# Kernel tuning notes

Measured on AMD Instinct MI355X. Metric: run time of the kernel, lower is better.

## Reference

```python
import jax, jax.numpy as jnp
import numpy as np

N_NODES = 100000


def gcn_conv(x, W, b, src, tgt, n_nodes):
    """PyG GCNConv: add self-loops, symmetric deg^-1/2 normalization, then aggregate."""
    xw = x @ W  # [N, out]
    # degree including self-loop (edge weights are all 1)
    deg = jnp.zeros((n_nodes,), dtype=x.dtype).at[tgt].add(1.0) + 1.0
    dinv = deg ** -0.5
    norm = dinv[src] * dinv[tgt]  # [E]
    agg = jax.ops.segment_sum(xw[src] * norm[:, None], tgt, num_segments=n_nodes)
    # self-loop contribution: norm_ii = dinv_i^2
    return agg + xw * (dinv ** 2)[:, None] + b


def setup_inputs() -> dict:
    key = jax.random.key(0)
    ks = jax.random.split(key, 9)
    d_in, d_hid, d_out = 128, 128, 64
    x = jax.random.normal(ks[0], (N_NODES, d_in), dtype=jnp.float32)
    edge_index = jax.random.randint(ks[1], (2, 200000), 0, N_NODES)
    pos_edge_index = jax.random.randint(ks[2], (2, 500000), 0, N_NODES)
    s = lambda k, shape, fan: jax.random.normal(k, shape, dtype=jnp.float32) / np.sqrt(fan)
    return {
        "x": x,
        "edge_index": edge_index,
        "pos_edge_index": pos_edge_index,
        "W_init": s(ks[3], (d_in, d_in), d_in),
        "b_init": jnp.zeros((d_in,), dtype=jnp.float32),
        "W1": s(ks[4], (d_in, d_hid), d_in),
        "b1": jnp.zeros((d_hid,), dtype=jnp.float32),
        "W2": s(ks[5], (d_hid, d_out), d_hid),
        "b2": jnp.zeros((d_out,), dtype=jnp.float32),
    }


def reference(x, edge_index, pos_edge_index, W_init, b_init, W1, b1, W2, b2):
    n = x.shape[0]
    src, tgt = pos_edge_index[0], pos_edge_index[1]
    h = x @ W_init + b_init                      # init_linear
    h = gcn_conv(h, W1, b1, src, tgt, n)         # conv1
    h = jax.nn.relu(h)
    h = gcn_conv(h, W2, b2, src, tgt, n)         # conv2
    # edge dot-product scoring (use_bilinear=False)
    logits = jnp.sum(h[edge_index[0]] * h[edge_index[1]], axis=-1)  # [E_pred]
    return logits
```

## Files before the change

### kernel.cpp

```cpp
#include <hip/hip_runtime.h>


typedef __attribute__((ext_vector_type(8))) short short8;
typedef __attribute__((ext_vector_type(4))) float f32x4;

__device__ __forceinline__ ushort f2bf(float v) {
    unsigned u = __float_as_uint(v);
    return (ushort)((u + 0x7FFFu + ((u >> 16) & 1u)) >> 16);
}
__device__ __forceinline__ float bf2f(ushort b) {
    return __uint_as_float(((unsigned)b) << 16);
}
__device__ __forceinline__ float bflo(unsigned u) { return __uint_as_float(u << 16); }
__device__ __forceinline__ float bfhi(unsigned u) { return __uint_as_float(u & 0xFFFF0000u); }
__device__ __forceinline__ unsigned packbf(float x, float y) {
    return (unsigned)f2bf(x) | ((unsigned)f2bf(y) << 16);
}
__device__ __forceinline__ void split2(float v, ushort& h, ushort& l) {
    unsigned u = __float_as_uint(v);
    unsigned hb = (u + 0x7FFFu + ((u >> 16) & 1u)) & 0xFFFF0000u;
    h = (ushort)(hb >> 16);
    l = f2bf(v - __uint_as_float(hb));
}

__global__ void prep_kernel(const float* __restrict__ Wi, const float* __restrict__ W1,
                            const float* __restrict__ W2,
                            ushort* __restrict__ Ti, ushort* __restrict__ T1,
                            ushort* __restrict__ T2, int* __restrict__ zp, int ztot)
{
    int o = blockIdx.x * blockDim.x + threadIdx.x;
    if (o < ztot) zp[o] = 0;
    if (o < 16384) {
        int c = o >> 7, k = o & 127;
        Ti[o] = f2bf(Wi[(size_t)k * 128 + c]);
    } else if (o < 32768) {
        int p = o - 16384;
        int c = p >> 7, k = p & 127;
        T1[p] = f2bf(W1[(size_t)k * 128 + c]);
    } else if (o < 40960) {
        int p = o - 32768;
        int c = p >> 7, k = p & 127;
        T2[p] = f2bf(W2[(size_t)k * 64 + c]);
    }
}

__global__ void hist_kernel(const int* __restrict__ tgt, int* __restrict__ counts, int e) {
    int i = blockIdx.x * blockDim.x + threadIdx.x;
    if (i < e) atomicAdd(&counts[tgt[i]], 1);
}
__global__ __launch_bounds__(256)
void scan1_kernel(const int* __restrict__ counts, int* __restrict__ rowptr,
                  int* __restrict__ bsum, float* __restrict__ dinv, int n)
{
    __shared__ int sdata[256];
    const int t = threadIdx.x;
    const int base = blockIdx.x * 1024 + t * 4;
    int v[4];
#pragma unroll
    for (int i = 0; i < 4; i++) v[i] = (base + i < n) ? counts[base + i] : 0;
#pragma unroll
    for (int i = 0; i < 4; i++)
        if (base + i < n) dinv[base + i] = 1.0f / sqrtf((float)(v[i] + 1));
    int tsum = v[0] + v[1] + v[2] + v[3];
    sdata[t] = tsum;
    __syncthreads();
    for (int off = 1; off < 256; off <<= 1) {
        int x = (t >= off) ? sdata[t - off] : 0;
        __syncthreads();
        if (t >= off) sdata[t] += x;
        __syncthreads();
    }
    if (t == 255) bsum[blockIdx.x] = sdata[255];
    int run = sdata[t] - tsum;
#pragma unroll
    for (int i = 0; i < 4; i++) {
        if (base + i < n) rowptr[base + i] = run;
        run += v[i];
    }
}
__global__ __launch_bounds__(256)
void scan2_kernel(int* __restrict__ bsum, int nb)
{
    __shared__ int sdata[256];
    const int t = threadIdx.x;
    int v = (t < nb) ? bsum[t] : 0;
    sdata[t] = v;
    __syncthreads();
    for (int off = 1; off < 256; off <<= 1) {
        int x = (t >= off) ? sdata[t - off] : 0;
        __syncthreads();
        if (t >= off) sdata[t] += x;
        __syncthreads();
    }
    if (t < nb) bsum[t] = sdata[t] - v;
}
__global__ void scan3_kernel(int* __restrict__ rowptr, const int* __restrict__ bsum,
                             int n, int e_total)
{
    int i = blockIdx.x * blockDim.x + threadIdx.x;
    if (i < n) rowptr[i] += bsum[i >> 10];
    if (i == 0) rowptr[n] = e_total;
}
__global__ void scatter_kernel(const int* __restrict__ src, const int* __restrict__ tgt,
                               const float* __restrict__ dinv, const int* __restrict__ rowptr,
                               int* __restrict__ cursor, int2* __restrict__ ew, int e)
{
    int i = blockIdx.x * blockDim.x + threadIdx.x;
    if (i >= e) return;
    int s = src[i], t = tgt[i];
    int p = rowptr[t] + atomicAdd(&cursor[t], 1);
    ew[p] = make_int2(s, __float_as_int(dinv[s] * dinv[t]));
}

__global__ __launch_bounds__(256)
void fused_gemm01_kernel(const float* __restrict__ x,
                         const ushort* __restrict__ WTi, const ushort* __restrict__ WT1,
                         const float* __restrict__ bias, ushort* __restrict__ xw1, int M)
{
    __shared__ ushort raw[20480];
    ushort (*H0)[128][8] = (ushort(*)[128][8])raw;
    ushort (*Ah)[128][8] = (ushort(*)[128][8])raw;
    ushort (*Al)[128][8] = (ushort(*)[128][8])(raw + 4096);
    ushort (*Bs)[128][8] = (ushort(*)[128][8])(raw + 16384);

    const int tid = threadIdx.x;
    const int row0 = blockIdx.x * 128;
    const int wv = tid >> 6;
    const int l  = tid & 63;
    const int lr = l & 15;
    const int lk = l >> 4;

    f32x4 acc0[8], acc1[8];
#pragma unroll
    for (int n = 0; n < 8; ++n) {
        acc0[n] = (f32x4){0.f, 0.f, 0.f, 0.f};
        acc1[n] = (f32x4){0.f, 0.f, 0.f, 0.f};
    }

    for (int kk = 0; kk < 128; kk += 32) {
        {
            const int r  = tid >> 1;
            const int kh = tid & 1;
            const int gr = row0 + r;
            float f[16];
            if (gr < M) {
                const float4* p = (const float4*)(x + (size_t)gr * 128 + kk + kh * 16);
                float4 q0 = p[0], q1 = p[1], q2 = p[2], q3 = p[3];
                f[0]=q0.x; f[1]=q0.y; f[2]=q0.z; f[3]=q0.w;
                f[4]=q1.x; f[5]=q1.y; f[6]=q1.z; f[7]=q1.w;
                f[8]=q2.x; f[9]=q2.y; f[10]=q2.z; f[11]=q2.w;
                f[12]=q3.x; f[13]=q3.y; f[14]=q3.z; f[15]=q3.w;
            } else {
#pragma unroll
                for (int j = 0; j < 16; j++) f[j] = 0.f;
            }
#pragma unroll
            for (int uu = 0; uu < 2; ++uu) {
                short8 hv, lv;
#pragma unroll
                for (int j = 0; j < 8; ++j) {
                    ushort h, lo;
                    split2(f[8 * uu + j], h, lo);
                    hv[j] = (short)h; lv[j] = (short)lo;
                }
                *(short8*)&Ah[2 * kh + uu][r][0] = hv;
                *(short8*)&Al[2 * kh + uu][r][0] = lv;
            }
        }
        {
#pragma unroll
            for (int u = 0; u < 2; ++u) {
                const int unit = tid * 2 + u;
                const int c   = unit >> 2;
                const int kgl = unit & 3;
                *(short8*)&Bs[kgl][c][0] = *(const short8*)(WTi + (size_t)c * 128 + kk + 8 * kgl);
            }
        }
        __syncthreads();
        short8 ah0 = *(const short8*)&Ah[lk][wv * 32 + lr][0];
        short8 ah1 = *(const short8*)&Ah[lk][wv * 32 + 16 + lr][0];
        short8 al0 = *(const short8*)&Al[lk][wv * 32 + lr][0];
        short8 al1 = *(const short8*)&Al[lk][wv * 32 + 16 + lr][0];
#pragma unroll
        for (int n = 0; n < 8; ++n) {
            short8 bh = *(const short8*)&Bs[lk][n * 16 + lr][0];
            acc0[n] = __builtin_amdgcn_mfma_f32_16x16x32_bf16(bh, ah0, acc0[n], 0, 0, 0);
            acc1[n] = __builtin_amdgcn_mfma_f32_16x16x32_bf16(bh, ah1, acc1[n], 0, 0, 0);
            acc0[n] = __builtin_amdgcn_mfma_f32_16x16x32_bf16(bh, al0, acc0[n], 0, 0, 0);
            acc1[n] = __builtin_amdgcn_mfma_f32_16x16x32_bf16(bh, al1, acc1[n], 0, 0, 0);
        }
        __syncthreads();
    }

#pragma unroll
    for (int n = 0; n < 8; ++n) {
        const float4 b4 = *(const float4*)(bias + n * 16 + 4 * lk);
        const float bb[4] = {b4.x, b4.y, b4.z, b4.w};
        const int ks = 2 * n + (lk >> 1);
        const int jo = (lk & 1) * 4;
#pragma unroll
        for (int half = 0; half < 2; ++half) {
            const int m = wv * 32 + 16 * half + lr;
            unsigned hw[4];
#pragma unroll
            for (int r = 0; r < 4; ++r)
                hw[r] = f2bf((half ? acc1[n][r] : acc0[n][r]) + bb[r]);
            uint2 uh;
            uh.x = hw[0] | (hw[1] << 16);
            uh.y = hw[2] | (hw[3] << 16);
            *(uint2*)&H0[ks][m][jo] = uh;
        }
    }
    __syncthreads();

#pragma unroll
    for (int n = 0; n < 8; ++n) {
        acc0[n] = (f32x4){0.f, 0.f, 0.f, 0.f};
        acc1[n] = (f32x4){0.f, 0.f, 0.f, 0.f};
    }
    for (int kk = 0; kk < 4; ++kk) {
        {
#pragma unroll
            for (int u = 0; u < 2; ++u) {
                const int unit = tid * 2 + u;
                const int c   = unit >> 2;
                const int kgl = unit & 3;
                *(short8*)&Bs[kgl][c][0] = *(const short8*)(WT1 + (size_t)c * 128 + kk * 32 + 8 * kgl);
            }
        }
        __syncthreads();
        short8 a0 = *(const short8*)&H0[kk * 4 + lk][wv * 32 + lr][0];
        short8 a1 = *(const short8*)&H0[kk * 4 + lk][wv * 32 + 16 + lr][0];
#pragma unroll
        for (int n = 0; n < 8; ++n) {
            short8 bh = *(const short8*)&Bs[lk][n * 16 + lr][0];
            acc0[n] = __builtin_amdgcn_mfma_f32_16x16x32_bf16(bh, a0, acc0[n], 0, 0, 0);
            acc1[n] = __builtin_amdgcn_mfma_f32_16x16x32_bf16(bh, a1, acc1[n], 0, 0, 0);
        }
        __syncthreads();
    }

#pragma unroll
    for (int n = 0; n < 8; ++n) {
#pragma unroll
        for (int half = 0; half < 2; ++half) {
            const int m = row0 + wv * 32 + 16 * half + lr;
            if (m < M) {
                uint2 u;
                const f32x4 a = half ? acc1[n] : acc0[n];
                u.x = (unsigned)f2bf(a[0]) | ((unsigned)f2bf(a[1]) << 16);
                u.y = (unsigned)f2bf(a[2]) | ((unsigned)f2bf(a[3]) << 16);
                *(uint2*)(xw1 + (size_t)m * 128 + n * 16 + 4 * lk) = u;
            }
        }
    }
}

__device__ __forceinline__ void tile_add(unsigned* p, float ax, float ay) {
    unsigned old = *p;
    *p = packbf(bflo(old) + ax, bfhi(old) + ay);
}

__global__ __launch_bounds__(256)
void conv1_fused_kernel(const ushort* __restrict__ xw1, const float* __restrict__ dinv,
                        const int* __restrict__ rowptr, const int2* __restrict__ ew,
                        const float* __restrict__ b1, const ushort* __restrict__ WT2,
                        ushort* __restrict__ xw2, int N)
{
    __shared__ ushort tile[16][65][8];
    __shared__ int srp[65];

    const int tid  = threadIdx.x;
    const int n0   = blockIdx.x * 64;
    const int nc   = min(64, N - n0);
    const int wv   = tid >> 6;
    const int lane = tid & 63;

    if (tid <= nc) srp[tid] = rowptr[n0 + tid];

    const float bb0 = b1[2 * lane];
    const float bb1 = b1[2 * lane + 1];
    const int  kg = lane >> 2;
    const int  jj = (2 * lane) & 7;
    unsigned* tbase = (unsigned*)&tile[kg][0][jj];
    for (int r = wv; r < 64; r += 4) {
        float vx = 0.f, vy = 0.f;
        if (r < nc) {
            unsigned u = *(const unsigned*)(xw1 + (size_t)(n0 + r) * 128 + 2 * lane);
            float dt = dinv[n0 + r];
            float cc = dt * dt;
            vx = fmaf(bflo(u), cc, bb0);
            vy = fmaf(bfhi(u), cc, bb1);
        }
        tbase[r * 4] = packbf(vx, vy);
    }
    __syncthreads();

    const int nlo = wv * 16;
    if (nlo < nc) {
        const int nhi = min(nlo + 16, nc);
        const int e0 = srp[0];
        int i = srp[nlo] - e0;
        const int iend = srp[nhi] - e0;
        int cur = nlo;
        int nxt = srp[nlo + 1] - e0;
        float ax = 0.f, ay = 0.f;

        for (; i + 16 <= iend; i += 16) {
            const int ib = __builtin_amdgcn_readfirstlane(e0 + i);
            int2 d[16];
#pragma unroll
            for (int u = 0; u < 16; ++u) d[u] = ew[ib + u];
            unsigned v[16];
#pragma unroll
            for (int u = 0; u < 16; ++u)
                v[u] = *(const unsigned*)(xw1 + (size_t)d[u].x * 128 + 2 * lane);
#pragma unroll
            for (int u = 0; u < 16; ++u) {
                const int idx = i + u;
                while (idx >= nxt) {
                    tile_add(tbase + cur * 4, ax, ay);
                    ax = 0.f; ay = 0.f;
                    ++cur;
                    nxt = srp[cur + 1] - e0;
                }
                const float w = __int_as_float(d[u].y);
                ax = fmaf(bflo(v[u]), w, ax);
                ay = fmaf(bfhi(v[u]), w, ay);
            }
        }
        for (; i + 4 <= iend; i += 4) {
            const int ib = __builtin_amdgcn_readfirstlane(e0 + i);
            int2 d[4];
#pragma unroll
            for (int u = 0; u < 4; ++u) d[u] = ew[ib + u];
            unsigned v[4];
#pragma unroll
            for (int u = 0; u < 4; ++u)
                v[u] = *(const unsigned*)(xw1 + (size_t)d[u].x * 128 + 2 * lane);
#pragma unroll
            for (int u = 0; u < 4; ++u) {
                const int idx = i + u;
                while (idx >= nxt) {
                    tile_add(tbase + cur * 4, ax, ay);
                    ax = 0.f; ay = 0.f;
                    ++cur;
                    nxt = srp[cur + 1] - e0;
                }
                const float w = __int_as_float(d[u].y);
                ax = fmaf(bflo(v[u]), w, ax);
                ay = fmaf(bfhi(v[u]), w, ay);
            }
        }
        for (; i < iend; ++i) {
            int2 d = ew[e0 + i];
            unsigned v = *(const unsigned*)(xw1 + (size_t)d.x * 128 + 2 * lane);
            while (i >= nxt) {
                tile_add(tbase + cur * 4, ax, ay);
                ax = 0.f; ay = 0.f;
                ++cur;
                nxt = srp[cur + 1] - e0;
            }
            const float w = __int_as_float(d.y);
            ax = fmaf(bflo(v), w, ax);
            ay = fmaf(bfhi(v), w, ay);
        }
        tile_add(tbase + cur * 4, ax, ay);
    }
    __syncthreads();

    const int lr = lane & 15;
    const int lk = lane >> 4;
    f32x4 acc[4];
#pragma unroll
    for (int n = 0; n < 4; ++n) acc[n] = (f32x4){0.f, 0.f, 0.f, 0.f};

    for (int kt = 0; kt < 4; ++kt) {
        short8 ah = *(const short8*)&tile[kt * 4 + lk][wv * 16 + lr][0];
#pragma unroll
        for (int j = 0; j < 8; ++j) {
            ushort vv = (ushort)ah[j];
            ah[j] = (short)((vv & 0x8000u) ? 0 : vv);
        }
#pragma unroll
        for (int n = 0; n < 4; ++n) {
            short8 bh = *(const short8*)(WT2 + (size_t)(n * 16 + lr) * 128 + kt * 32 + lk * 8);
            acc[n] = __builtin_amdgcn_mfma_f32_16x16x32_bf16(bh, ah, acc[n], 0, 0, 0);
        }
    }

    const int ml = wv * 16 + lr;
    if (ml < nc) {
        const size_t m = (size_t)(n0 + ml);
#pragma unroll
        for (int n = 0; n < 4; ++n) {
            uint2 u;
            u.x = (unsigned)f2bf(acc[n][0]) | ((unsigned)f2bf(acc[n][1]) << 16);
            u.y = (unsigned)f2bf(acc[n][2]) | ((unsigned)f2bf(acc[n][3]) << 16);
            *(uint2*)(xw2 + m * 64 + n * 16 + 4 * lk) = u;
        }
    }
}

__global__ __launch_bounds__(256)
void gather2_flat_kernel(const ushort* __restrict__ xw, const float* __restrict__ dinv,
                         const int* __restrict__ rowptr, const int2* __restrict__ ew,
                         const float* __restrict__ bias, ushort* __restrict__ out, int N)
{
    __shared__ int srp[65];

    const int tid  = threadIdx.x;
    const int n0   = blockIdx.x * 64;
    const int nc   = min(64, N - n0);
    const int wv   = tid >> 6;
    const int lane = tid & 63;

    if (tid <= nc) srp[tid] = rowptr[n0 + tid];
    __syncthreads();

    const int nlo = wv * 16;
    if (nlo >= nc) return;
    const int nhi = min(nlo + 16, nc);
    const float bl = bias[lane];

    int j = srp[nlo];
    const int jend = srp[nhi];
    int cur = nlo;
    int nxt = srp[nlo + 1];
    float acc = 0.f;

    auto flush = [&](int c, float a) {
        const size_t g = (size_t)(n0 + c);
        const float self = bf2f(xw[g * 64 + lane]);
        const float dt = dinv[g];
        out[g * 64 + lane] = f2bf(fmaf(self, dt * dt, a + bl));
    };

    for (; j + 16 <= jend; j += 16) {
        const int jb = __builtin_amdgcn_readfirstlane(j);
        int2 d[16];
#pragma unroll
        for (int u = 0; u < 16; ++u) d[u] = ew[jb + u];
        float v[16];
#pragma unroll
        for (int u = 0; u < 16; ++u) v[u] = bf2f(xw[(size_t)d[u].x * 64 + lane]);
#pragma unroll
        for (int u = 0; u < 16; ++u) {
            const int idx = j + u;
            while (idx >= nxt) {
                flush(cur, acc);
                acc = 0.f;
                ++cur;
                nxt = srp[cur + 1];
            }
            acc = fmaf(v[u], __int_as_float(d[u].y), acc);
        }
    }
    for (; j + 4 <= jend; j += 4) {
        const int jb = __builtin_amdgcn_readfirstlane(j);
        int2 d[4];
#pragma unroll
        for (int u = 0; u < 4; ++u) d[u] = ew[jb + u];
        float v[4];
#pragma unroll
        for (int u = 0; u < 4; ++u) v[u] = bf2f(xw[(size_t)d[u].x * 64 + lane]);
#pragma unroll
        for (int u = 0; u < 4; ++u) {
            const int idx = j + u;
            while (idx >= nxt) {
                flush(cur, acc);
                acc = 0.f;
                ++cur;
                nxt = srp[cur + 1];
            }
            acc = fmaf(v[u], __int_as_float(d[u].y), acc);
        }
    }
    for (; j < jend; ++j) {
        int2 d = ew[j];
        float v = bf2f(xw[(size_t)d.x * 64 + lane]);
        while (j >= nxt) {
            flush(cur, acc);
            acc = 0.f;
            ++cur;
            nxt = srp[cur + 1];
        }
        acc = fmaf(v, __int_as_float(d.y), acc);
    }
    flush(cur, acc);
    for (int c = cur + 1; c < nhi; ++c) flush(c, 0.f);
}

__global__ void score_kernel(const ushort* __restrict__ h, const int* __restrict__ ea,
                             const int* __restrict__ eb, float* __restrict__ out, int E)
{
    long long gid = (long long)blockIdx.x * blockDim.x + threadIdx.x;
    int e = (int)(gid >> 2);
    int l = (int)(gid & 3);
    if (e >= E) return;
    int a = ea[e], b = eb[e];
    const uint4* pa = (const uint4*)(h + (size_t)a * 64 + 16 * l);
    const uint4* pb = (const uint4*)(h + (size_t)b * 64 + 16 * l);
    uint4 ua0 = pa[0], ua1 = pa[1];
    uint4 ub0 = pb[0], ub1 = pb[1];
    float s;
    s  = bflo(ua0.x) * bflo(ub0.x) + bfhi(ua0.x) * bfhi(ub0.x);
    s += bflo(ua0.y) * bflo(ub0.y) + bfhi(ua0.y) * bfhi(ub0.y);
    s += bflo(ua0.z) * bflo(ub0.z) + bfhi(ua0.z) * bfhi(ub0.z);
    s += bflo(ua0.w) * bflo(ub0.w) + bfhi(ua0.w) * bfhi(ub0.w);
    s += bflo(ua1.x) * bflo(ub1.x) + bfhi(ua1.x) * bfhi(ub1.x);
    s += bflo(ua1.y) * bflo(ub1.y) + bfhi(ua1.y) * bfhi(ub1.y);
    s += bflo(ua1.z) * bflo(ub1.z) + bfhi(ua1.z) * bfhi(ub1.z);
    s += bflo(ua1.w) * bflo(ub1.w) + bfhi(ua1.w) * bfhi(ub1.w);
    s += __shfl_xor(s, 2);
    s += __shfl_xor(s, 1);
    if (l == 0) out[e] = s;
}

extern "C" void kernel_launch(void* const* d_in, const int* in_sizes, int n_in,
                              void* d_out, int out_size, void* d_ws, size_t ws_size,
                              hipStream_t stream)
{
    const float* x              = (const float*)d_in[0];
    const int*   edge_index     = (const int*)d_in[1];
    const int*   pos_edge_index = (const int*)d_in[2];
    const float* W_init         = (const float*)d_in[3];
    const float* b_init         = (const float*)d_in[4];
    const float* W1             = (const float*)d_in[5];
    const float* b1             = (const float*)d_in[6];
    const float* W2             = (const float*)d_in[7];
    const float* b2             = (const float*)d_in[8];
    float* out = (float*)d_out;

    const int N     = in_sizes[0] / 128;
    const int Epred = in_sizes[1] / 2;
    const int E     = in_sizes[2] / 2;

    const int* src = pos_edge_index;
    const int* tgt = pos_edge_index + E;
    const int* ea  = edge_index;
    const int* eb  = edge_index + Epred;

    int2*   ew   = (int2*)d_ws;
    ushort* regA = (ushort*)(ew + E);
    ushort* regB = regA + (size_t)N * 128;
    float*  dinv = (float*)(regB + (size_t)N * 128);
    int*   counts = (int*)(dinv + N);
    int*   cursor = counts + N;
    int*   rowptr = cursor + N;
    int*   bsum   = rowptr + N + 2;
    ushort* WTi = (ushort*)(((uintptr_t)(bsum + 256) + 15) & ~(uintptr_t)15);
    ushort* WT1 = WTi + 16384;
    ushort* WT2 = WT1 + 16384;

    ushort* xw1 = regA;
    ushort* xw2 = regB;
    ushort* h2  = regB + (size_t)N * 64;

    const int BLK = 256;
    const int nb  = (N + 1023) / 1024;

    prep_kernel<<<(2 * N + BLK - 1) / BLK, BLK, 0, stream>>>(
        W_init, W1, W2, WTi, WT1, WT2, counts, 2 * N);

    hist_kernel<<<(E + BLK - 1) / BLK, BLK, 0, stream>>>(tgt, counts, E);
    scan1_kernel<<<nb, 256, 0, stream>>>(counts, rowptr, bsum, dinv, N);
    scan2_kernel<<<1, 256, 0, stream>>>(bsum, nb);
    scan3_kernel<<<(N + BLK - 1) / BLK, BLK, 0, stream>>>(rowptr, bsum, N, E);
    scatter_kernel<<<(E + BLK - 1) / BLK, BLK, 0, stream>>>(src, tgt, dinv, rowptr, cursor, ew, E);

    fused_gemm01_kernel<<<(N + 127) / 128, BLK, 0, stream>>>(x, WTi, WT1, b_init, xw1, N);

    conv1_fused_kernel<<<(N + 63) / 64, BLK, 0, stream>>>(
        xw1, dinv, rowptr, ew, b1, WT2, xw2, N);

    gather2_flat_kernel<<<(N + 63) / 64, BLK, 0, stream>>>(
        xw2, dinv, rowptr, ew, b2, h2, N);

    score_kernel<<<((long long)Epred * 4 + BLK - 1) / BLK, BLK, 0, stream>>>(
        h2, ea, eb, out, Epred);
}
```

Before: 164.5 us.

## Halve nodes per block in conv kernels and fold block-sum scan into fixup

Conv1 and gather2 now process 32 nodes per block instead of 64, so each wave handles 8 nodes and the MFMA stage splits the 32x64 output across four waves by row and column group. This doubles the grid size to improve load balance and latency hiding on the irregular gather. Separately, the single-block scan2 launch is removed: each scan3 block has one thread serially sum the preceding block totals, trading one launch for redundant serial reads of up to about a hundred values.

```diff
diff --git a/kernel.cpp b/kernel.cpp
--- a/kernel.cpp
+++ b/kernel.cpp
@@ -78,27 +78,19 @@
         run += v[i];
     }
 }
-__global__ __launch_bounds__(256)
-void scan2_kernel(int* __restrict__ bsum, int nb)
-{
-    __shared__ int sdata[256];
-    const int t = threadIdx.x;
-    int v = (t < nb) ? bsum[t] : 0;
-    sdata[t] = v;
+__global__ void scan3_kernel(int* __restrict__ rowptr, const int* __restrict__ bsum,
+                             int n, int e_total, int nb)
+{
+    __shared__ int pre;
+    const int k0 = (blockIdx.x * 256) >> 10;
+    if (threadIdx.x == 0) {
+        int s = 0;
+        for (int k = 0; k < k0; ++k) s += bsum[k];
+        pre = s;
+    }
     __syncthreads();
-    for (int off = 1; off < 256; off <<= 1) {
-        int x = (t >= off) ? sdata[t - off] : 0;
-        __syncthreads();
-        if (t >= off) sdata[t] += x;
-        __syncthreads();
-    }
-    if (t < nb) bsum[t] = sdata[t] - v;
-}
-__global__ void scan3_kernel(int* __restrict__ rowptr, const int* __restrict__ bsum,
-                             int n, int e_total)
-{
-    int i = blockIdx.x * blockDim.x + threadIdx.x;
-    if (i < n) rowptr[i] += bsum[i >> 10];
+    int i = blockIdx.x * 256 + threadIdx.x;
+    if (i < n) rowptr[i] += pre;
     if (i == 0) rowptr[n] = e_total;
 }
 __global__ void scatter_kernel(const int* __restrict__ src, const int* __restrict__ tgt,
@@ -267,12 +259,12 @@
                         const float* __restrict__ b1, const ushort* __restrict__ WT2,
                         ushort* __restrict__ xw2, int N)
 {
-    __shared__ ushort tile[16][65][8];
-    __shared__ int srp[65];
+    __shared__ ushort tile[16][33][8];
+    __shared__ int srp[33];
 
     const int tid  = threadIdx.x;
-    const int n0   = blockIdx.x * 64;
-    const int nc   = min(64, N - n0);
+    const int n0   = blockIdx.x * 32;
+    const int nc   = min(32, N - n0);
     const int wv   = tid >> 6;
     const int lane = tid & 63;
 
@@ -283,7 +275,7 @@
     const int  kg = lane >> 2;
     const int  jj = (2 * lane) & 7;
     unsigned* tbase = (unsigned*)&tile[kg][0][jj];
-    for (int r = wv; r < 64; r += 4) {
+    for (int r = wv; r < 32; r += 4) {
         float vx = 0.f, vy = 0.f;
         if (r < nc) {
             unsigned u = *(const unsigned*)(xw1 + (size_t)(n0 + r) * 128 + 2 * lane);
@@ -296,9 +288,9 @@
     }
     __syncthreads();
 
-    const int nlo = wv * 16;
+    const int nlo = wv * 8;
     if (nlo < nc) {
-        const int nhi = min(nlo + 16, nc);
+        const int nhi = min(nlo + 8, nc);
         const int e0 = srp[0];
         int i = srp[nlo] - e0;
         const int iend = srp[nhi] - e0;
@@ -371,32 +363,36 @@
 
     const int lr = lane & 15;
     const int lk = lane >> 4;
-    f32x4 acc[4];
-#pragma unroll
-    for (int n = 0; n < 4; ++n) acc[n] = (f32x4){0.f, 0.f, 0.f, 0.f};
+    const int rowg = wv & 1;
+    const int colg = wv >> 1;
+    f32x4 acc[2];
+    acc[0] = (f32x4){0.f, 0.f, 0.f, 0.f};
+    acc[1] = (f32x4){0.f, 0.f, 0.f, 0.f};
 
     for (int kt = 0; kt < 4; ++kt) {
-        short8 ah = *(const short8*)&tile[kt * 4 + lk][wv * 16 + lr][0];
+        short8 ah = *(const short8*)&tile[kt * 4 + lk][rowg * 16 + lr][0];
 #pragma unroll
         for (int j = 0; j < 8; ++j) {
             ushort vv = (ushort)ah[j];
             ah[j] = (short)((vv & 0x8000u) ? 0 : vv);
         }
 #pragma unroll
-        for (int n = 0; n < 4; ++n) {
+        for (int nn = 0; nn < 2; ++nn) {
+            const int n = colg * 2 + nn;
             short8 bh = *(const short8*)(WT2 + (size_t)(n * 16 + lr) * 128 + kt * 32 + lk * 8);
-            acc[n] = __builtin_amdgcn_mfma_f32_16x16x32_bf16(bh, ah, acc[n], 0, 0, 0);
-        }
-    }
-
-    const int ml = wv * 16 + lr;
+            acc[nn] = __builtin_amdgcn_mfma_f32_16x16x32_bf16(bh, ah, acc[nn], 0, 0, 0);
+        }
+    }
+
+    const int ml = rowg * 16 + lr;
     if (ml < nc) {
         const size_t m = (size_t)(n0 + ml);
 #pragma unroll
-        for (int n = 0; n < 4; ++n) {
+        for (int nn = 0; nn < 2; ++nn) {
+            const int n = colg * 2 + nn;
             uint2 u;
-            u.x = (unsigned)f2bf(acc[n][0]) | ((unsigned)f2bf(acc[n][1]) << 16);
-            u.y = (unsigned)f2bf(acc[n][2]) | ((unsigned)f2bf(acc[n][3]) << 16);
+            u.x = (unsigned)f2bf(acc[nn][0]) | ((unsigned)f2bf(acc[nn][1]) << 16);
+            u.y = (unsigned)f2bf(acc[nn][2]) | ((unsigned)f2bf(acc[nn][3]) << 16);
             *(uint2*)(xw2 + m * 64 + n * 16 + 4 * lk) = u;
         }
     }
@@ -407,20 +403,20 @@
                          const int* __restrict__ rowptr, const int2* __restrict__ ew,
                          const float* __restrict__ bias, ushort* __restrict__ out, int N)
 {
-    __shared__ int srp[65];
+    __shared__ int srp[33];
 
     const int tid  = threadIdx.x;
-    const int n0   = blockIdx.x * 64;
-    const int nc   = min(64, N - n0);
+    const int n0   = blockIdx.x * 32;
+    const int nc   = min(32, N - n0);
     const int wv   = tid >> 6;
     const int lane = tid & 63;
 
     if (tid <= nc) srp[tid] = rowptr[n0 + tid];
     __syncthreads();
 
-    const int nlo = wv * 16;
+    const int nlo = wv * 8;
     if (nlo >= nc) return;
-    const int nhi = min(nlo + 16, nc);
+    const int nhi = min(nlo + 8, nc);
     const float bl = bias[lane];
 
     int j = srp[nlo];
@@ -565,16 +561,15 @@
 
     hist_kernel<<<(E + BLK - 1) / BLK, BLK, 0, stream>>>(tgt, counts, E);
     scan1_kernel<<<nb, 256, 0, stream>>>(counts, rowptr, bsum, dinv, N);
-    scan2_kernel<<<1, 256, 0, stream>>>(bsum, nb);
-    scan3_kernel<<<(N + BLK - 1) / BLK, BLK, 0, stream>>>(rowptr, bsum, N, E);
+    scan3_kernel<<<(N + BLK - 1) / BLK, BLK, 0, stream>>>(rowptr, bsum, N, E, nb);
     scatter_kernel<<<(E + BLK - 1) / BLK, BLK, 0, stream>>>(src, tgt, dinv, rowptr, cursor, ew, E);
 
     fused_gemm01_kernel<<<(N + 127) / 128, BLK, 0, stream>>>(x, WTi, WT1, b_init, xw1, N);
 
-    conv1_fused_kernel<<<(N + 63) / 64, BLK, 0, stream>>>(
+    conv1_fused_kernel<<<(N + 31) / 32, BLK, 0, stream>>>(
         xw1, dinv, rowptr, ew, b1, WT2, xw2, N);
 
-    gather2_flat_kernel<<<(N + 63) / 64, BLK, 0, stream>>>(
+    gather2_flat_kernel<<<(N + 31) / 32, BLK, 0, stream>>>(
         xw2, dinv, rowptr, ew, b2, h2, N);
 
     score_kernel<<<((long long)Epred * 4 + BLK - 1) / BLK, BLK, 0, stream>>>(
```

Result: no change. 165.4 us (+0.5%).
